# Kernel optimization log

Hardware: AMD Instinct MI355X
Metric: run time of the kernel (lower is better)

## Reference

```python
import jax, jax.numpy as jnp
import numpy as np

N = 50000   # nodes
C = 128     # in == hidden == out channels (required by residual add)
E = 500000  # edges (before self-loops)
H = 64      # hidden width of pos_nn / attn_nn


def setup_inputs() -> dict:
    key = jax.random.key(0)
    ks = jax.random.split(key, 20)
    s = lambda fan_in: 1.0 / np.sqrt(fan_in)
    d = {}
    d["x"] = jax.random.normal(ks[0], (N, C), jnp.float32)
    d["pos"] = jax.random.uniform(ks[1], (N, 3), jnp.float32)
    d["edge_index"] = jax.random.randint(ks[2], (2, E), 0, N, dtype=jnp.int32)
    # lin_in / lin_out (with bias)
    d["W_in"] = jax.random.normal(ks[3], (C, C), jnp.float32) * s(C)
    d["b_in"] = jnp.zeros((C,), jnp.float32)
    d["W_out"] = jax.random.normal(ks[4], (C, C), jnp.float32) * s(C)
    d["b_out"] = jnp.zeros((C,), jnp.float32)
    # PointTransformerConv internal linears (bias=False in PyG)
    d["W_lin"] = jax.random.normal(ks[5], (C, C), jnp.float32) * s(C)
    d["W_src"] = jax.random.normal(ks[6], (C, C), jnp.float32) * s(C)
    d["W_dst"] = jax.random.normal(ks[7], (C, C), jnp.float32) * s(C)
    # pos_nn: Lin(3,64) -> ReLU -> Lin(64,C)
    d["Wp1"] = jax.random.normal(ks[8], (3, H), jnp.float32) * s(3)
    d["bp1"] = jnp.zeros((H,), jnp.float32)
    d["Wp2"] = jax.random.normal(ks[9], (H, C), jnp.float32) * s(H)
    d["bp2"] = jnp.zeros((C,), jnp.float32)
    # attn_nn: Lin(C,64) -> ReLU -> Lin(64,C)
    d["Wa1"] = jax.random.normal(ks[10], (C, H), jnp.float32) * s(C)
    d["ba1"] = jnp.zeros((H,), jnp.float32)
    d["Wa2"] = jax.random.normal(ks[11], (H, C), jnp.float32) * s(H)
    d["ba2"] = jnp.zeros((C,), jnp.float32)
    return d


def reference(x, pos, edge_index, W_in, b_in, W_out, b_out, W_lin, W_src, W_dst,
              Wp1, bp1, Wp2, bp2, Wa1, ba1, Wa2, ba2):
    n = x.shape[0]
    x_skip = x
    h = jax.nn.relu(x @ W_in + b_in)                      # lin_in + relu, [N,C]
    # PointTransformerConv with add_self_loops=True
    loop = jnp.arange(n, dtype=edge_index.dtype)
    src = jnp.concatenate([edge_index[0], loop])          # j (source)
    dst = jnp.concatenate([edge_index[1], loop])          # i (target)
    a_src = h @ W_src                                      # lin_src(x), [N,C]
    a_dst = h @ W_dst                                      # lin_dst(x), [N,C]
    v = h @ W_lin                                          # lin(x),     [N,C]
    rel = pos[dst] - pos[src]                              # pos_i - pos_j, [Et,3]
    delta = jax.nn.relu(rel @ Wp1 + bp1) @ Wp2 + bp2       # pos_nn, [Et,C]
    alpha = a_dst[dst] - a_src[src] + delta                # alpha_i - alpha_j + delta
    alpha = jax.nn.relu(alpha @ Wa1 + ba1) @ Wa2 + ba2     # attn_nn, [Et,C]
    # per-destination, per-channel softmax over edges
    amax = jax.ops.segment_max(alpha, dst, num_segments=n)
    amax = jnp.where(jnp.isfinite(amax), amax, 0.0)
    ex = jnp.exp(alpha - amax[dst])
    den = jax.ops.segment_sum(ex, dst, num_segments=n) + 1e-16
    w = ex / den[dst]
    out = jax.ops.segment_sum(w * (v[src] + delta), dst, num_segments=n)  # [N,C]
    out = jax.nn.relu(out @ W_out + b_out)                 # lin_out + relu
    return out + x_skip
```

## Files before the change

### kernel.cpp

```cpp
#include <hip/hip_runtime.h>

typedef _Float16 h2_t __attribute__((ext_vector_type(2)));
typedef _Float16 f16x4v __attribute__((ext_vector_type(4)));
typedef _Float16 f16x8 __attribute__((ext_vector_type(8)));
typedef float f32x4 __attribute__((ext_vector_type(4)));

struct F8pair { f16x4v lo, hi; };
static __device__ __forceinline__ f16x8 ldfrag(const _Float16* p) {
    F8pair r;
    r.lo = *(const f16x4v*)p;
    r.hi = *(const f16x4v*)(p + 4);
    return __builtin_bit_cast(f16x8, r);
}

static __device__ __forceinline__ unsigned int pkrtz(float a, float b) {
    return __builtin_bit_cast(unsigned int, __builtin_amdgcn_cvt_pkrtz(a, b));
}

static __device__ __forceinline__ float h2lo(unsigned int w) {
    h2_t h = __builtin_bit_cast(h2_t, w);
    return (float)h.x;
}
static __device__ __forceinline__ float h2hi(unsigned int w) {
    h2_t h = __builtin_bit_cast(h2_t, w);
    return (float)h.y;
}

static __device__ __forceinline__ f16x8 mkfrag(const float* p) {
    float4 a = ((const float4*)p)[0];
    float4 b = ((const float4*)p)[1];
    uint4 u;
    u.x = pkrtz(a.x, a.y); u.y = pkrtz(a.z, a.w);
    u.z = pkrtz(b.x, b.y); u.w = pkrtz(b.z, b.w);
    return __builtin_bit_cast(f16x8, u);
}

__global__ void k_pre(const float* __restrict__ W_src, const float* __restrict__ W_dst,
                      const float* __restrict__ Wa1, const float* __restrict__ ba1,
                      const float* __restrict__ Wp2, const float* __restrict__ bp2,
                      const float* __restrict__ Wa2, const float* __restrict__ W_in,
                      const float* __restrict__ W_lin, const float* __restrict__ W_out,
                      float* __restrict__ bias2, _Float16* __restrict__ Wcat,
                      _Float16* __restrict__ Wnode, _Float16* __restrict__ WoutT)
{
    int idx = blockIdx.x * 256 + threadIdx.x;
    if (idx < 64) {
        int l = idx;
        float a = ba1[l];
        for (int c = 0; c < 128; ++c) a = fmaf(bp2[c], Wa1[c*64+l], a);
        bias2[l] = a;
    } else if (idx < 64 + 21760) {
        int j = idx - 64;
        int row = j / 68, k = j % 68;
        float val = 0.f;
        if (k < 64) {
            if (row < 64) {
                int Q = 2 * (row & 31) + (row >> 5);
                float a = 0.f;
                for (int c = 0; c < 128; ++c) a = fmaf(Wp2[k*128+c], Wa1[c*64+Q], a);
                val = a;
            } else if (row < 192) {
                int cpos = row - 64;
                int P = 2 * (cpos & 63) + (cpos >> 6);
                val = Wp2[k*128 + P];
            } else {
                int cpos = row - 192;
                int P = 2 * (cpos & 63) + (cpos >> 6);
                int Qk = 2 * (k & 31) + (k >> 5);
                val = Wa2[Qk*128 + P];
            }
        }
        Wcat[j] = (_Float16)val;
    } else if (idx < 21824 + 16896) {
        int j = idx - 21824;
        int c = j / 132, k = j % 132;
        Wnode[j] = (_Float16)((k < 128) ? W_in[k*128+c] : 0.f);
    } else if (idx < 38720 + 16896) {
        int j = idx - 38720;
        int c = j / 132, k = j % 132;
        Wnode[16896 + j] = (_Float16)((k < 128) ? W_lin[k*128+c] : 0.f);
    } else if (idx < 55616 + 16896) {
        int j = idx - 55616;
        int c = j / 132, k = j % 132;
        float val = 0.f;
        if (k < 128) {
            if (c < 64) {
                for (int q = 0; q < 128; ++q) val = fmaf(W_src[k*128+q], Wa1[q*64+c], val);
            } else {
                for (int q = 0; q < 128; ++q) val = fmaf(W_dst[k*128+q], Wa1[q*64+(c-64)], val);
            }
        }
        Wnode[33792 + j] = (_Float16)val;
    } else if (idx < 72512 + 16896) {
        int j = idx - 72512;
        int c = j / 132, k = j % 132;
        WoutT[j] = (_Float16)((k < 128) ? W_out[k*128+c] : 0.f);
    }
}

__global__ void k_zero(int* __restrict__ p, int n) {
    int i = blockIdx.x * 256 + threadIdx.x;
    if (i < n) p[i] = 0;
}

__global__ void k_count(const int* __restrict__ ei, int E, int N, int* __restrict__ cnt) {
    int i = blockIdx.x * 256 + threadIdx.x;
    int T = E + N;
    if (i >= T) return;
    int dst = (i < E) ? ei[E + i] : (i - E);
    atomicAdd(&cnt[dst], 1);
}

__global__ void k_pos4(const float* __restrict__ pos, float4* __restrict__ pos4, int N) {
    int i = blockIdx.x * 256 + threadIdx.x;
    if (i < N) pos4[i] = make_float4(pos[3*i], pos[3*i+1], pos[3*i+2], 0.f);
}

__global__ __launch_bounds__(1024) void k_scan1(int* __restrict__ cnt, int* __restrict__ bsum, int N) {
    __shared__ int sc[1024];
    int t = threadIdx.x;
    int i = blockIdx.x * 1024 + t;
    int val = (i < N) ? cnt[i] : 0;
    sc[t] = val;
    __syncthreads();
    for (int off = 1; off < 1024; off <<= 1) {
        int tmp = (t >= off) ? sc[t - off] : 0;
        __syncthreads();
        sc[t] += tmp;
        __syncthreads();
    }
    int incl = sc[t];
    if (i < N) cnt[i] = incl - val;
    if (t == 1023) bsum[blockIdx.x] = incl;
}

__global__ void k_scan2(int* __restrict__ bsum, int* __restrict__ offs, int nb, int N) {
    if (threadIdx.x == 0 && blockIdx.x == 0) {
        int run = 0;
        for (int i = 0; i < nb; ++i) { int tv = bsum[i]; bsum[i] = run; run += tv; }
        offs[N] = run;
    }
}

__global__ void k_scan3(int* __restrict__ offs, const int* __restrict__ bsum,
                        int* __restrict__ cursor, int N) {
    int i = blockIdx.x * 256 + threadIdx.x;
    if (i < N) {
        int o = offs[i] + bsum[i >> 10];
        offs[i] = o;
        cursor[i] = o;
    }
}

__global__ void k_scatter(const int* __restrict__ ei, int E, int N,
                          int* __restrict__ cursor, int* __restrict__ srcs) {
    int i = blockIdx.x * 256 + threadIdx.x;
    int T = E + N;
    if (i >= T) return;
    int s_, d_;
    if (i < E) { s_ = ei[i]; d_ = ei[E + i]; }
    else       { s_ = i - E; d_ = i - E; }
    int p = atomicAdd(&cursor[d_], 1);
    srcs[p] = s_;
}

__global__ __launch_bounds__(512) void k_node2(
    const float* __restrict__ x, const float* __restrict__ b_in,
    const float* __restrict__ bp2, const _Float16* __restrict__ Wnode,
    unsigned int* __restrict__ vpk, unsigned int* __restrict__ pspk,
    unsigned int* __restrict__ pdpk, int N, int nTiles, int nWavesTot)
{
    __shared__ _Float16 WB[3 * 16896];
    __shared__ _Float16 HT[8][16 * 132];
    int tid = threadIdx.x;
    {
        const unsigned int* g = (const unsigned int*)Wnode;
        unsigned int* s = (unsigned int*)WB;
        for (int i = tid; i < 3 * 16896 / 2; i += 512) s[i] = g[i];
    }
    __syncthreads();

    int wid = tid >> 6, lane = tid & 63;
    int l15 = lane & 15, akg = lane >> 4;
    _Float16* ht = HT[wid];

    int gw = blockIdx.x * 8 + wid;
    for (int t = gw; t < nTiles; t += nWavesTot) {
        int row0 = t * 16;
        int rowa = row0 + l15; if (rowa > N - 1) rowa = N - 1;

        f16x8 A[4];
        #pragma unroll
        for (int f = 0; f < 4; ++f)
            A[f] = mkfrag(&x[(size_t)rowa * 128 + f * 32 + akg * 8]);

        #pragma unroll
        for (int ct = 0; ct < 8; ++ct) {
            const _Float16* bb = &WB[(ct * 16 + l15) * 132];
            f32x4 d = {0.f, 0.f, 0.f, 0.f};
            #pragma unroll
            for (int f = 0; f < 4; ++f)
                d = __builtin_amdgcn_mfma_f32_16x16x32_f16(A[f], ldfrag(bb + f * 32 + akg * 8), d, 0, 0, 0);
            float bin = b_in[ct * 16 + l15];
            #pragma unroll
            for (int j = 0; j < 4; ++j)
                ht[(akg * 4 + j) * 132 + ct * 16 + l15] = (_Float16)fmaxf(d[j] + bin, 0.f);
        }

        f16x8 H[4];
        #pragma unroll
        for (int f = 0; f < 4; ++f)
            H[f] = ldfrag(&ht[l15 * 132 + f * 32 + akg * 8]);

        #pragma unroll
        for (int ct = 0; ct < 8; ++ct) {
            const _Float16* bb = &WB[16896 + (ct * 16 + l15) * 132];
            f32x4 d = {0.f, 0.f, 0.f, 0.f};
            #pragma unroll
            for (int f = 0; f < 4; ++f)
                d = __builtin_amdgcn_mfma_f32_16x16x32_f16(H[f], ldfrag(bb + f * 32 + akg * 8), d, 0, 0, 0);
            float bp = bp2[ct * 16 + l15];
            #pragma unroll
            for (int j = 0; j < 4; ++j) {
                float val = d[j] + bp;
                float partner = __shfl_xor(val, 1);
                int row = row0 + akg * 4 + j;
                if (((l15 & 1) == 0) && row < N)
                    vpk[(size_t)row * 64 + ct * 8 + (l15 >> 1)] = pkrtz(val, partner);
            }
        }

        #pragma unroll
        for (int ct = 0; ct < 8; ++ct) {
            const _Float16* bb = &WB[33792 + (ct * 16 + l15) * 132];
            f32x4 d = {0.f, 0.f, 0.f, 0.f};
            #pragma unroll
            for (int f = 0; f < 4; ++f)
                d = __builtin_amdgcn_mfma_f32_16x16x32_f16(H[f], ldfrag(bb + f * 32 + akg * 8), d, 0, 0, 0);
            #pragma unroll
            for (int j = 0; j < 4; ++j) {
                float val = d[j];
                float partner = __shfl_xor(val, 1);
                int row = row0 + akg * 4 + j;
                if (((l15 & 1) == 0) && row < N) {
                    if (ct < 4)
                        pspk[(size_t)row * 32 + ct * 8 + (l15 >> 1)] = pkrtz(val, partner);
                    else
                        pdpk[(size_t)row * 32 + (ct - 4) * 8 + (l15 >> 1)] = pkrtz(val, partner);
                }
            }
        }
    }
}

__global__ __launch_bounds__(512, 2) void k_edge(
    const unsigned int* __restrict__ vpk, const unsigned int* __restrict__ pspk,
    const unsigned int* __restrict__ pdpk,
    const float4* __restrict__ pos4, const int* __restrict__ srcs,
    const int* __restrict__ offs, const _Float16* __restrict__ Wcat,
    const float* __restrict__ Wp1, const float* __restrict__ bp1,
    const float* __restrict__ bias2,
    float* __restrict__ out, int N, int nWavesTot)
{
    __shared__ _Float16 WL[320 * 68];
    __shared__ _Float16 PH[8][16 * 68];
    int tid = threadIdx.x;
    {
        const unsigned int* g = (const unsigned int*)Wcat;
        unsigned int* s = (unsigned int*)WL;
        for (int i = tid; i < 320 * 68 / 2; i += 512) s[i] = g[i];
    }
    __syncthreads();

    int wid = tid >> 6, lane = tid & 63;
    int l15 = lane & 15, akg = lane >> 4;
    _Float16* ph  = PH[wid];
    _Float16* ahv = ph;

    float wp10 = Wp1[lane], wp11 = Wp1[64 + lane], wp12 = Wp1[128 + lane], bp1l = bp1[lane];
    float bias2_r[4];
    #pragma unroll
    for (int nt = 0; nt < 4; ++nt)
        bias2_r[nt] = bias2[2 * ((nt & 1) * 16 + l15) + (nt >> 1)];

    int gw = blockIdx.x * 8 + wid;
    for (int node = gw; node < N; node += nWavesTot) {
        int beg = offs[node], end = offs[node + 1];
        float4 pi = pos4[node];
        unsigned int pdw0 = pdpk[(size_t)node * 32 + l15];
        unsigned int pdw1 = pdpk[(size_t)node * 32 + 16 + l15];
        float base4[4];
        #pragma unroll
        for (int nt = 0; nt < 4; ++nt) {
            unsigned int wd = (nt & 1) ? pdw1 : pdw0;
            base4[nt] = ((nt >> 1) ? h2hi(wd) : h2lo(wd)) + bias2_r[nt];
        }

        float rn[8], rd[8];
        #pragma unroll
        for (int nt = 0; nt < 8; ++nt) { rn[nt] = 0.f; rd[nt] = 0.f; }

        for (int e0 = beg; e0 < end; e0 += 16) {
            int ei_ = e0 + l15;
            int eim = (ei_ < end) ? ei_ : (end - 1);
            int s16 = srcs[eim];
            float4 pj = pos4[s16];
            if (akg == 0) {
                uint2 rr;
                rr.x = pkrtz(pi.x - pj.x, pi.y - pj.y);
                rr.y = pkrtz(pi.z - pj.z, 0.f);
                *(uint2*)&ph[l15 * 68 + 64] = rr;
            }
            #pragma unroll
            for (int ee = 0; ee < 16; ++ee) {
                uint2 rr = *(const uint2*)&ph[ee * 68 + 64];
                float rx = h2lo(rr.x), ry = h2hi(rr.x), rz = h2lo(rr.y);
                float phv = fmaxf(fmaf(rx, wp10, fmaf(ry, wp11, fmaf(rz, wp12, bp1l))), 0.f);
                ph[ee * 68 + lane] = (_Float16)phv;
            }

            f16x8 A0 = ldfrag(&ph[l15 * 68 + akg * 8]);
            f16x8 A1 = ldfrag(&ph[l15 * 68 + 32 + akg * 8]);

            int se[4];
            #pragma unroll
            for (int j = 0; j < 4; ++j) se[j] = __shfl(s16, akg * 4 + j);

            {
                unsigned int psw0[4], psw1[4];
                #pragma unroll
                for (int j = 0; j < 4; ++j) {
                    psw0[j] = pspk[(size_t)se[j] * 32 + l15];
                    psw1[j] = pspk[(size_t)se[j] * 32 + 16 + l15];
                }
                #pragma unroll
                for (int nt = 0; nt < 4; ++nt) {
                    const _Float16* br = &WL[(nt * 16 + l15) * 68];
                    f16x8 B0 = ldfrag(br + akg * 8);
                    f16x8 B1 = ldfrag(br + 32 + akg * 8);
                    f32x4 a = {0.f, 0.f, 0.f, 0.f};
                    a = __builtin_amdgcn_mfma_f32_16x16x32_f16(A0, B0, a, 0, 0, 0);
                    a = __builtin_amdgcn_mfma_f32_16x16x32_f16(A1, B1, a, 0, 0, 0);
                    #pragma unroll
                    for (int j = 0; j < 4; ++j) {
                        unsigned int ws = (nt & 1) ? psw1[j] : psw0[j];
                        float psv = (nt >> 1) ? h2hi(ws) : h2lo(ws);
                        float ahf = fmaxf(a[j] + base4[nt] - psv, 0.f);
                        ahv[(akg * 4 + j) * 68 + nt * 16 + l15] = (_Float16)ahf;
                    }
                }
            }

            f16x8 C0 = ldfrag(&ahv[l15 * 68 + akg * 8]);
            f16x8 C1 = ldfrag(&ahv[l15 * 68 + 32 + akg * 8]);

            #pragma unroll
            for (int hf = 0; hf < 2; ++hf) {
                unsigned int wvA[4], wvB[4];
                #pragma unroll
                for (int j = 0; j < 4; ++j) {
                    wvA[j] = vpk[(size_t)se[j] * 64 + hf * 32 + l15];
                    wvB[j] = vpk[(size_t)se[j] * 64 + hf * 32 + 16 + l15];
                }
                #pragma unroll
                for (int q = 0; q < 4; ++q) {
                    int nt = (q & 1) + hf * 2 + (q >> 1) * 4;
                    const _Float16* br2 = &WL[(64 + nt * 16 + l15) * 68];
                    f16x8 B20 = ldfrag(br2 + akg * 8);
                    f16x8 B21 = ldfrag(br2 + 32 + akg * 8);
                    f32x4 a2 = {0.f, 0.f, 0.f, 0.f};
                    a2 = __builtin_amdgcn_mfma_f32_16x16x32_f16(A0, B20, a2, 0, 0, 0);
                    a2 = __builtin_amdgcn_mfma_f32_16x16x32_f16(A1, B21, a2, 0, 0, 0);
                    const _Float16* br3 = &WL[(192 + nt * 16 + l15) * 68];
                    f16x8 B30 = ldfrag(br3 + akg * 8);
                    f16x8 B31 = ldfrag(br3 + 32 + akg * 8);
                    f32x4 a3 = {0.f, 0.f, 0.f, 0.f};
                    a3 = __builtin_amdgcn_mfma_f32_16x16x32_f16(C0, B30, a3, 0, 0, 0);
                    a3 = __builtin_amdgcn_mfma_f32_16x16x32_f16(C1, B31, a3, 0, 0, 0);
                    #pragma unroll
                    for (int j = 0; j < 4; ++j) {
                        bool vj = (e0 + akg * 4 + j) < end;
                        unsigned int wv = (q & 1) ? wvB[j] : wvA[j];
                        float vv = (q >> 1) ? h2hi(wv) : h2lo(wv);
                        float alpha = vj ? a3[j] : -1e30f;
                        float wexp = __expf(fminf(alpha, 60.f));
                        float u = vv + a2[j];
                        rd[nt] += wexp;
                        rn[nt] = fmaf(wexp, u, rn[nt]);
                    }
                }
            }
        }

        #pragma unroll
        for (int nt = 0; nt < 8; ++nt) {
            rn[nt] += __shfl_xor(rn[nt], 16);
            rn[nt] += __shfl_xor(rn[nt], 32);
            rd[nt] += __shfl_xor(rd[nt], 16);
            rd[nt] += __shfl_xor(rd[nt], 32);
        }
        if (akg == 0) {
            #pragma unroll
            for (int nt2 = 0; nt2 < 4; ++nt2) {
                float2 o;
                o.x = rn[nt2]     / (rd[nt2]     + 1e-16f);
                o.y = rn[nt2 + 4] / (rd[nt2 + 4] + 1e-16f);
                ((float2*)out)[(size_t)node * 64 + nt2 * 16 + l15] = o;
            }
        }
    }
}

__global__ __launch_bounds__(256) void k_out2(
    const float* __restrict__ x, const float* __restrict__ b_out,
    const _Float16* __restrict__ WoutT, float* __restrict__ out,
    int N, int nTiles, int nWavesTot)
{
    __shared__ _Float16 WB[16896];
    int tid = threadIdx.x;
    {
        const unsigned int* g = (const unsigned int*)WoutT;
        unsigned int* s = (unsigned int*)WB;
        for (int i = tid; i < 16896 / 2; i += 256) s[i] = g[i];
    }
    __syncthreads();

    int wid = tid >> 6, lane = tid & 63;
    int l15 = lane & 15, akg = lane >> 4;

    int gw = blockIdx.x * 4 + wid;
    for (int t = gw; t < nTiles; t += nWavesTot) {
        int row0 = t * 16;
        int rowa = row0 + l15; if (rowa > N - 1) rowa = N - 1;

        f16x8 A[4];
        #pragma unroll
        for (int f = 0; f < 4; ++f)
            A[f] = mkfrag(&out[(size_t)rowa * 128 + f * 32 + akg * 8]);

        #pragma unroll
        for (int ct = 0; ct < 8; ++ct) {
            const _Float16* bb = &WB[(ct * 16 + l15) * 132];
            f32x4 d = {0.f, 0.f, 0.f, 0.f};
            #pragma unroll
            for (int f = 0; f < 4; ++f)
                d = __builtin_amdgcn_mfma_f32_16x16x32_f16(A[f], ldfrag(bb + f * 32 + akg * 8), d, 0, 0, 0);
            float bo = b_out[ct * 16 + l15];
            #pragma unroll
            for (int j = 0; j < 4; ++j) {
                int row = row0 + akg * 4 + j;
                if (row < N) {
                    int c = ct * 16 + l15;
                    out[(size_t)row * 128 + c] = fmaxf(d[j] + bo, 0.f) + x[(size_t)row * 128 + c];
                }
            }
        }
    }
}

extern "C" void kernel_launch(void* const* d_in, const int* in_sizes, int n_in,
                              void* d_out, int out_size, void* d_ws, size_t ws_size,
                              hipStream_t stream)
{
    const float* x     = (const float*)d_in[0];
    const float* pos   = (const float*)d_in[1];
    const int*   ei    = (const int*)d_in[2];
    const float* W_in  = (const float*)d_in[3];
    const float* b_in  = (const float*)d_in[4];
    const float* W_out = (const float*)d_in[5];
    const float* b_out = (const float*)d_in[6];
    const float* W_lin = (const float*)d_in[7];
    const float* W_src = (const float*)d_in[8];
    const float* W_dst = (const float*)d_in[9];
    const float* Wp1   = (const float*)d_in[10];
    const float* bp1   = (const float*)d_in[11];
    const float* Wp2   = (const float*)d_in[12];
    const float* bp2   = (const float*)d_in[13];
    const float* Wa1   = (const float*)d_in[14];
    const float* ba1   = (const float*)d_in[15];
    const float* Wa2   = (const float*)d_in[16];
    const float* ba2   = (const float*)d_in[17];
    (void)ba2;

    int N = in_sizes[0] / 128;
    int E = in_sizes[2] / 2;
    int T = E + N;
    int nTiles = (N + 15) / 16;
    float* out = (float*)d_out;

    char* w = (char*)d_ws;
    auto alloc = [&](size_t bytes) -> char* {
        char* p = w;
        w += (bytes + 255) & ~(size_t)255;
        return p;
    };
    unsigned int* vpk  = (unsigned int*)alloc((size_t)N * 64 * 4);
    unsigned int* pspk = (unsigned int*)alloc((size_t)N * 32 * 4);
    unsigned int* pdpk = (unsigned int*)alloc((size_t)N * 32 * 4);
    float4* pos4 = (float4*)alloc((size_t)N * 16);
    float* bias2 = (float*)alloc(64 * 4);
    _Float16* Wcat  = (_Float16*)alloc(21760 * 2);
    _Float16* Wnode = (_Float16*)alloc(3 * 16896 * 2);
    _Float16* WoutT = (_Float16*)alloc(16896 * 2);
    int*   offs  = (int*)alloc((size_t)(N + 1) * 4);
    int*   cursor= (int*)alloc((size_t)N * 4);
    int*   bsum  = (int*)alloc(256 * 4);
    int*   srcs  = (int*)alloc((size_t)T * 4);

    k_pre<<<dim3((89408 + 255) / 256), dim3(256), 0, stream>>>(
        W_src, W_dst, Wa1, ba1, Wp2, bp2, Wa2, W_in, W_lin, W_out,
        bias2, Wcat, Wnode, WoutT);
    k_zero<<<dim3((N + 1 + 255) / 256), dim3(256), 0, stream>>>(offs, N + 1);
    k_count<<<dim3((T + 255) / 256), dim3(256), 0, stream>>>(ei, E, N, offs);
    k_pos4<<<dim3((N + 255) / 256), dim3(256), 0, stream>>>(pos, pos4, N);
    int nb = (N + 1023) / 1024;
    k_scan1<<<dim3(nb), dim3(1024), 0, stream>>>(offs, bsum, N);
    k_scan2<<<dim3(1), dim3(64), 0, stream>>>(bsum, offs, nb, N);
    k_scan3<<<dim3((N + 255) / 256), dim3(256), 0, stream>>>(offs, bsum, cursor, N);
    k_scatter<<<dim3((T + 255) / 256), dim3(256), 0, stream>>>(ei, E, N, cursor, srcs);

    int nodeBlocks = 192;
    k_node2<<<dim3(nodeBlocks), dim3(512), 0, stream>>>(x, b_in, bp2, Wnode,
                                                        vpk, pspk, pdpk, N, nTiles,
                                                        nodeBlocks * 8);
    int nWavesTot = 8192;
    k_edge<<<dim3(1024), dim3(512), 0, stream>>>(vpk, pspk, pdpk, pos4, srcs, offs, Wcat,
                                                 Wp1, bp1, bias2,
                                                 out, N, nWavesTot);
    int outBlocks = 256;
    k_out2<<<dim3(outBlocks), dim3(256), 0, stream>>>(x, b_out, WoutT, out, N, nTiles,
                                                      outBlocks * 4);
}
```

Before: 334.6 us.

## Split each node's edge work across two waves by output channel half

Each destination node is now processed by two waves, each handling half of the output channels in the attention/value stage. The grid is doubled and the launch-bounds occupancy hint is dropped. This raises parallelism and cuts per-wave accumulator registers. In exchange, the positional MLP, first attention layer and edge gathers are done twice per node, and LDS occupancy may limit the extra waves.

```diff
diff --git a/kernel.cpp b/kernel.cpp
--- a/kernel.cpp
+++ b/kernel.cpp
@@ -253,14 +253,14 @@
     }
 }
 
-__global__ __launch_bounds__(512, 2) void k_edge(
+__global__ __launch_bounds__(512) void k_edge(
     const unsigned int* __restrict__ vpk, const unsigned int* __restrict__ pspk,
     const unsigned int* __restrict__ pdpk,
     const float4* __restrict__ pos4, const int* __restrict__ srcs,
     const int* __restrict__ offs, const _Float16* __restrict__ Wcat,
     const float* __restrict__ Wp1, const float* __restrict__ bp1,
     const float* __restrict__ bias2,
-    float* __restrict__ out, int N, int nWavesTot)
+    float* __restrict__ out, int N, int totWaves)
 {
     __shared__ _Float16 WL[320 * 68];
     __shared__ _Float16 PH[8][16 * 68];
@@ -284,7 +284,9 @@
         bias2_r[nt] = bias2[2 * ((nt & 1) * 16 + l15) + (nt >> 1)];
 
     int gw = blockIdx.x * 8 + wid;
-    for (int node = gw; node < N; node += nWavesTot) {
+    int half = gw & 1;
+    int nodeStride = totWaves >> 1;
+    for (int node = (gw >> 1); node < N; node += nodeStride) {
         int beg = offs[node], end = offs[node + 1];
         float4 pi = pos4[node];
         unsigned int pdw0 = pdpk[(size_t)node * 32 + l15];
@@ -296,9 +298,9 @@
             base4[nt] = ((nt >> 1) ? h2hi(wd) : h2lo(wd)) + bias2_r[nt];
         }
 
-        float rn[8], rd[8];
-        #pragma unroll
-        for (int nt = 0; nt < 8; ++nt) { rn[nt] = 0.f; rd[nt] = 0.f; }
+        float rn[4], rd[4];
+        #pragma unroll
+        for (int m = 0; m < 4; ++m) { rn[m] = 0.f; rd[m] = 0.f; }
 
         for (int e0 = beg; e0 < end; e0 += 16) {
             int ei_ = e0 + l15;
@@ -354,17 +356,16 @@
             f16x8 C0 = ldfrag(&ahv[l15 * 68 + akg * 8]);
             f16x8 C1 = ldfrag(&ahv[l15 * 68 + 32 + akg * 8]);
 
-            #pragma unroll
-            for (int hf = 0; hf < 2; ++hf) {
+            {
                 unsigned int wvA[4], wvB[4];
                 #pragma unroll
                 for (int j = 0; j < 4; ++j) {
-                    wvA[j] = vpk[(size_t)se[j] * 64 + hf * 32 + l15];
-                    wvB[j] = vpk[(size_t)se[j] * 64 + hf * 32 + 16 + l15];
+                    wvA[j] = vpk[(size_t)se[j] * 64 + half * 32 + l15];
+                    wvB[j] = vpk[(size_t)se[j] * 64 + half * 32 + 16 + l15];
                 }
                 #pragma unroll
                 for (int q = 0; q < 4; ++q) {
-                    int nt = (q & 1) + hf * 2 + (q >> 1) * 4;
+                    int nt = (q & 1) + half * 2 + (q >> 1) * 4;
                     const _Float16* br2 = &WL[(64 + nt * 16 + l15) * 68];
                     f16x8 B20 = ldfrag(br2 + akg * 8);
                     f16x8 B21 = ldfrag(br2 + 32 + akg * 8);
@@ -385,27 +386,27 @@
                         float alpha = vj ? a3[j] : -1e30f;
                         float wexp = __expf(fminf(alpha, 60.f));
                         float u = vv + a2[j];
-                        rd[nt] += wexp;
-                        rn[nt] = fmaf(wexp, u, rn[nt]);
+                        rd[q] += wexp;
+                        rn[q] = fmaf(wexp, u, rn[q]);
                     }
                 }
             }
         }
 
         #pragma unroll
-        for (int nt = 0; nt < 8; ++nt) {
-            rn[nt] += __shfl_xor(rn[nt], 16);
-            rn[nt] += __shfl_xor(rn[nt], 32);
-            rd[nt] += __shfl_xor(rd[nt], 16);
-            rd[nt] += __shfl_xor(rd[nt], 32);
+        for (int m = 0; m < 4; ++m) {
+            rn[m] += __shfl_xor(rn[m], 16);
+            rn[m] += __shfl_xor(rn[m], 32);
+            rd[m] += __shfl_xor(rd[m], 16);
+            rd[m] += __shfl_xor(rd[m], 32);
         }
         if (akg == 0) {
             #pragma unroll
-            for (int nt2 = 0; nt2 < 4; ++nt2) {
+            for (int d = 0; d < 2; ++d) {
                 float2 o;
-                o.x = rn[nt2]     / (rd[nt2]     + 1e-16f);
-                o.y = rn[nt2 + 4] / (rd[nt2 + 4] + 1e-16f);
-                ((float2*)out)[(size_t)node * 64 + nt2 * 16 + l15] = o;
+                o.x = rn[d]     / (rd[d]     + 1e-16f);
+                o.y = rn[d + 2] / (rd[d + 2] + 1e-16f);
+                ((float2*)out)[(size_t)node * 64 + (half * 2 + d) * 16 + l15] = o;
             }
         }
     }
@@ -523,10 +524,10 @@
     k_node2<<<dim3(nodeBlocks), dim3(512), 0, stream>>>(x, b_in, bp2, Wnode,
                                                         vpk, pspk, pdpk, N, nTiles,
                                                         nodeBlocks * 8);
-    int nWavesTot = 8192;
-    k_edge<<<dim3(1024), dim3(512), 0, stream>>>(vpk, pspk, pdpk, pos4, srcs, offs, Wcat,
+    int totWaves = 16384;
+    k_edge<<<dim3(2048), dim3(512), 0, stream>>>(vpk, pspk, pdpk, pos4, srcs, offs, Wcat,
                                                  Wp1, bp1, bias2,
-                                                 out, N, nWavesTot);
+                                                 out, N, totWaves);
     int outBlocks = 256;
     k_out2<<<dim3(outBlocks), dim3(256), 0, stream>>>(x, b_out, WoutT, out, N, nTiles,
                                                       outBlocks * 4);
```

Measured after the change: 360.6 us. +7.8%, slower.
